# Kernel tuning notes

Hardware: AMD Instinct MI355X
Metric: run time of the kernel (lower is better)

Reference implementation:

```python
import jax, jax.numpy as jnp
import numpy as np

N = 100000   # nodes
E = 500000   # edges
H = 128      # h_dim
TAU = 1.0    # gumbel-softmax temperature (module default)


def setup_inputs() -> dict:
    key = jax.random.key(0)
    k = jax.random.split(key, 6)
    h = jax.random.normal(k[0], (N, H), dtype=jnp.float32)
    W1 = jax.random.normal(k[1], (2 * H, H // 2), dtype=jnp.float32) / np.float32(np.sqrt(2 * H))
    b1 = jnp.zeros((H // 2,), dtype=jnp.float32)
    W2 = jax.random.normal(k[2], (H // 2, 1), dtype=jnp.float32) / np.float32(np.sqrt(H // 2))
    b2 = jnp.zeros((1,), dtype=jnp.float32)
    u = jax.random.uniform(k[3], (E, 2), dtype=jnp.float32, minval=1e-6, maxval=1.0)
    edge_index = jax.random.randint(k[4], (2, E), 0, N, dtype=jnp.int32)
    return {"h": h, "W1": W1, "b1": b1, "W2": W2, "b2": b2, "u": u, "edge_index": edge_index}


def reference(h, W1, b1, W2, b2, u, edge_index):
    row, col = edge_index[0], edge_index[1]
    # gather endpoint features and concat: [E, 2H]
    edge_feat = jnp.concatenate([h[row], h[col]], axis=-1)
    # 2-layer MLP scorer -> per-edge logit [E]
    hid = jax.nn.relu(edge_feat @ W1 + b1)
    logits = (hid @ W2 + b2)[:, 0]
    # binary gumbel-softmax over [keep-logit=0, logit]
    samp_logits = jnp.stack([jnp.zeros_like(logits), logits], axis=-1)  # [E, 2]
    g = -jnp.log(-jnp.log(u))  # gumbel noise from uniform
    y_soft = jax.nn.softmax((samp_logits + g) / TAU, axis=-1)
    # hard=True straight-through
    idx = jnp.argmax(y_soft, axis=-1)
    y_hard = jax.nn.one_hot(idx, 2, dtype=y_soft.dtype)
    y = y_hard - jax.lax.stop_gradient(y_soft) + y_soft
    weights = y[:, 1]
    return (weights, logits)
```

## Files before the change

kernel.cpp:

```cpp
#include <hip/hip_runtime.h>
#include <math.h>

#define NN 100000
#define NE 500000

__global__ __launch_bounds__(256)
void node_proj(const float* __restrict__ h, const float* __restrict__ W1,
               const float* __restrict__ b1, float* __restrict__ AB, int nnodes)
{
    __shared__ float lh[64 * 132];

    const int t   = threadIdx.x;
    const int tj  = t & 15;
    const int tnf = t >> 4;
    const int n0  = blockIdx.x * 64;

#pragma unroll
    for (int i = 0; i < 8; ++i) {
        int flat = i * 256 + t;
        int nl = flat >> 5;
        int c  = flat & 31;
        int ng = n0 + nl;
        float4 v = make_float4(0.f, 0.f, 0.f, 0.f);
        if (ng < nnodes) v = *(const float4*)&h[(size_t)ng * 128 + c * 4];
        *(float4*)&lh[nl * 132 + c * 4] = v;
    }
    __syncthreads();

    const float* wa_base = W1 + tj * 4;
    const float* wb_base = W1 + 128 * 64 + tj * 4;

    float acc[4][8];
    {
        float4 bv = *(const float4*)&b1[tj * 4];
#pragma unroll
        for (int r = 0; r < 4; ++r) {
            acc[r][0] = bv.x; acc[r][1] = bv.y; acc[r][2] = bv.z; acc[r][3] = bv.w;
            acc[r][4] = 0.f;  acc[r][5] = 0.f;  acc[r][6] = 0.f;  acc[r][7] = 0.f;
        }
    }

    float4 A0[4], B0[4], A1[4], B1[4];
#pragma unroll
    for (int kk = 0; kk < 4; ++kk) {
        A0[kk] = *(const float4*)&wa_base[kk * 64];
        B0[kk] = *(const float4*)&wb_base[kk * 64];
    }

#define LOAD_W(AX, BX, K4)                                              \
    _Pragma("unroll")                                                   \
    for (int kk = 0; kk < 4; ++kk) {                                    \
        AX[kk] = *(const float4*)&wa_base[((K4) * 4 + kk) * 64];        \
        BX[kk] = *(const float4*)&wb_base[((K4) * 4 + kk) * 64];        \
    }

#define COMPUTE(AX, BX, K4)                                             \
    {                                                                   \
        float4 hv[4];                                                   \
        _Pragma("unroll")                                               \
        for (int r = 0; r < 4; ++r)                                     \
            hv[r] = *(const float4*)&lh[(tnf + 16 * r) * 132 + (K4) * 4]; \
        _Pragma("unroll")                                               \
        for (int kk = 0; kk < 4; ++kk) {                                \
            float4 wa = AX[kk], wb = BX[kk];                            \
            _Pragma("unroll")                                           \
            for (int r = 0; r < 4; ++r) {                               \
                float hk = (kk == 0) ? hv[r].x : (kk == 1) ? hv[r].y    \
                         : (kk == 2) ? hv[r].z : hv[r].w;               \
                acc[r][0] += hk * wa.x;                                 \
                acc[r][1] += hk * wa.y;                                 \
                acc[r][2] += hk * wa.z;                                 \
                acc[r][3] += hk * wa.w;                                 \
                acc[r][4] += hk * wb.x;                                 \
                acc[r][5] += hk * wb.y;                                 \
                acc[r][6] += hk * wb.z;                                 \
                acc[r][7] += hk * wb.w;                                 \
            }                                                           \
        }                                                               \
    }

#pragma unroll 1
    for (int k4 = 0; k4 < 30; k4 += 2) {
        LOAD_W(A1, B1, k4 + 1)
        COMPUTE(A0, B0, k4)
        LOAD_W(A0, B0, k4 + 2)
        COMPUTE(A1, B1, k4 + 1)
    }
    LOAD_W(A1, B1, 31)
    COMPUTE(A0, B0, 30)
    COMPUTE(A1, B1, 31)

#undef LOAD_W
#undef COMPUTE

#pragma unroll
    for (int r = 0; r < 4; ++r) {
        int ng = n0 + tnf + 16 * r;
        if (ng >= nnodes) continue;
        float* orow = AB + (size_t)ng * 128;
        *(float4*)&orow[tj * 4]      = make_float4(acc[r][0], acc[r][1], acc[r][2], acc[r][3]);
        *(float4*)&orow[64 + tj * 4] = make_float4(acc[r][4], acc[r][5], acc[r][6], acc[r][7]);
    }
}

__global__ __launch_bounds__(256)
void edge_sample(const float* __restrict__ AB, const float* __restrict__ W2,
                 const float* __restrict__ b2, const float* __restrict__ u,
                 const int* __restrict__ ei, float* __restrict__ out)
{
    int t = threadIdx.x;
    int l = t & 15;
    int e = blockIdx.x * 16 + (t >> 4);

    int row = ei[e];
    int col = ei[NE + e];

    float4 a = *(const float4*)&AB[(size_t)row * 128 + l * 4];
    float4 b = *(const float4*)&AB[(size_t)col * 128 + 64 + l * 4];
    float4 w = *(const float4*)&W2[l * 4];

    float h0 = fmaxf(a.x + b.x, 0.f);
    float h1 = fmaxf(a.y + b.y, 0.f);
    float h2 = fmaxf(a.z + b.z, 0.f);
    float h3 = fmaxf(a.w + b.w, 0.f);

    float p = h0 * w.x + h1 * w.y + h2 * w.z + h3 * w.w;
    p += __shfl_xor(p, 1);
    p += __shfl_xor(p, 2);
    p += __shfl_xor(p, 4);
    p += __shfl_xor(p, 8);

    if (l == 0) {
        float logit = p + b2[0];
        float u0 = u[2 * e];
        float u1 = u[2 * e + 1];
        float g0 = -logf(-logf(u0));
        float g1 = -logf(-logf(u1));
        out[e]      = (logit + g1 > g0) ? 1.0f : 0.0f;
        out[NE + e] = logit;
    }
}

__global__ __launch_bounds__(256)
void edge_direct(const float* __restrict__ h, const float* __restrict__ W1,
                 const float* __restrict__ b1, const float* __restrict__ W2,
                 const float* __restrict__ b2, const float* __restrict__ u,
                 const int* __restrict__ ei, float* __restrict__ out)
{
    int t = threadIdx.x;
    int l = t & 15;
    int e = blockIdx.x * 16 + (t >> 4);

    int row = ei[e];
    int col = ei[NE + e];

    float a0 = 0.f, a1 = 0.f, a2 = 0.f, a3 = 0.f;
    const float* hr = h + (size_t)row * 128;
    const float* hc = h + (size_t)col * 128;

    for (int k4 = 0; k4 < 32; ++k4) {
        float4 hv = *(const float4*)&hr[k4 * 4];
#pragma unroll
        for (int kk = 0; kk < 4; ++kk) {
            float4 wr = *(const float4*)&W1[(k4 * 4 + kk) * 64 + l * 4];
            float hval = (&hv.x)[kk];
            a0 += hval * wr.x; a1 += hval * wr.y; a2 += hval * wr.z; a3 += hval * wr.w;
        }
    }
    for (int k4 = 0; k4 < 32; ++k4) {
        float4 hv = *(const float4*)&hc[k4 * 4];
#pragma unroll
        for (int kk = 0; kk < 4; ++kk) {
            float4 wr = *(const float4*)&W1[(128 + k4 * 4 + kk) * 64 + l * 4];
            float hval = (&hv.x)[kk];
            a0 += hval * wr.x; a1 += hval * wr.y; a2 += hval * wr.z; a3 += hval * wr.w;
        }
    }
    float4 bb = *(const float4*)&b1[l * 4];
    float4 w  = *(const float4*)&W2[l * 4];
    float h0 = fmaxf(a0 + bb.x, 0.f);
    float h1 = fmaxf(a1 + bb.y, 0.f);
    float h2 = fmaxf(a2 + bb.z, 0.f);
    float h3 = fmaxf(a3 + bb.w, 0.f);

    float p = h0 * w.x + h1 * w.y + h2 * w.z + h3 * w.w;
    p += __shfl_xor(p, 1);
    p += __shfl_xor(p, 2);
    p += __shfl_xor(p, 4);
    p += __shfl_xor(p, 8);

    if (l == 0) {
        float logit = p + b2[0];
        float u0 = u[2 * e];
        float u1 = u[2 * e + 1];
        float g0 = -logf(-logf(u0));
        float g1 = -logf(-logf(u1));
        out[e]      = (logit + g1 > g0) ? 1.0f : 0.0f;
        out[NE + e] = logit;
    }
}

extern "C" void kernel_launch(void* const* d_in, const int* in_sizes, int n_in,
                              void* d_out, int out_size, void* d_ws, size_t ws_size,
                              hipStream_t stream)
{
    const float* h  = (const float*)d_in[0];
    const float* W1 = (const float*)d_in[1];
    const float* b1 = (const float*)d_in[2];
    const float* W2 = (const float*)d_in[3];
    const float* b2 = (const float*)d_in[4];
    const float* u  = (const float*)d_in[5];
    const int*   ei = (const int*)d_in[6];
    float* out = (float*)d_out;

    const size_t need = (size_t)NN * 128 * sizeof(float);
    if (ws_size >= need) {
        float* AB = (float*)d_ws;
        int nblocks = (NN + 63) / 64;
        node_proj<<<nblocks, 256, 0, stream>>>(h, W1, b1, AB, NN);
        edge_sample<<<NE / 16, 256, 0, stream>>>(AB, W2, b2, u, ei, out);
    } else {
        edge_direct<<<NE / 16, 256, 0, stream>>>(h, W1, b1, W2, b2, u, ei, out);
    }
}
```

Before: 104.6 us.

## Use bf16 MFMA for node projection with split weights and fp32 fallback near threshold

Replaces the fp32 node projection with a bf16 MFMA kernel: W1 is prepacked into high/low bf16 halves in MFMA fragment layout, while h is truncated to bf16. To guard the hard sample decision against the resulting error, the edge kernel recomputes the logit in full fp32 from h whenever the decision margin is under 0.02. This adds a prepack launch and divergent recompute work on borderline edges. The logits output is left with bf16-level error on most edges, which could break a tight tolerance.

```diff
diff --git a/kernel.cpp b/kernel.cpp
--- a/kernel.cpp
+++ b/kernel.cpp
@@ -3,6 +3,173 @@
 
 #define NN 100000
 #define NE 500000
+
+typedef short bf16x8 __attribute__((ext_vector_type(8)));
+typedef float f32x4  __attribute__((ext_vector_type(4)));
+
+static __device__ __forceinline__ unsigned short f2bf_rne(float x) {
+    unsigned int u = __builtin_bit_cast(unsigned int, x);
+    unsigned int r = u + 0x7fffu + ((u >> 16) & 1u);
+    return (unsigned short)(r >> 16);
+}
+static __device__ __forceinline__ float bf2f(unsigned short b) {
+    return __builtin_bit_cast(float, (unsigned int)b << 16);
+}
+
+__global__ __launch_bounds__(256)
+void prepack_w(const float* __restrict__ W1, unsigned short* __restrict__ WPh,
+               unsigned short* __restrict__ WPl)
+{
+    int idx = blockIdx.x * 256 + threadIdx.x;
+    int e  = idx & 7;
+    int l  = (idx >> 3) & 63;
+    int kt = (idx >> 9) & 3;
+    int jt = idx >> 11;
+    int k = kt * 32 + (l >> 4) * 8 + e;
+    int j = jt * 16 + (l & 15);
+    float w = (j < 64) ? W1[k * 64 + j] : W1[(128 + k) * 64 + (j - 64)];
+    unsigned short hb = f2bf_rne(w);
+    unsigned short lb = f2bf_rne(w - bf2f(hb));
+    WPh[idx] = hb;
+    WPl[idx] = lb;
+}
+
+__global__ __launch_bounds__(256)
+void mfma_proj(const float* __restrict__ h, const unsigned short* __restrict__ WPh,
+               const unsigned short* __restrict__ WPl, const float* __restrict__ b1,
+               float* __restrict__ AB, int nnodes)
+{
+    const int t  = threadIdx.x;
+    const int wv = t >> 6;
+    const int l  = t & 63;
+    const int lr = l & 15;
+    const int q  = l >> 4;
+    const int n0 = blockIdx.x * 64 + wv * 16;
+    const int arow = n0 + lr;
+    const bool aval = (arow < nnodes);
+
+    bf16x8 ah[4];
+    const float* hrow = h + (size_t)arow * 128;
+#pragma unroll
+    for (int kt = 0; kt < 4; ++kt) {
+        float4 x0 = make_float4(0.f, 0.f, 0.f, 0.f);
+        float4 x1 = make_float4(0.f, 0.f, 0.f, 0.f);
+        if (aval) {
+            x0 = *(const float4*)&hrow[kt * 32 + q * 8];
+            x1 = *(const float4*)&hrow[kt * 32 + q * 8 + 4];
+        }
+        float xs[8] = {x0.x, x0.y, x0.z, x0.w, x1.x, x1.y, x1.z, x1.w};
+        union { bf16x8 v; unsigned short u[8]; } H;
+#pragma unroll
+        for (int e = 0; e < 8; ++e)
+            H.u[e] = (unsigned short)(__builtin_bit_cast(unsigned int, xs[e]) >> 16);
+        ah[kt] = H.v;
+    }
+
+    const int drow = n0 + q * 4;
+
+#pragma unroll
+    for (int jt = 0; jt < 8; ++jt) {
+        f32x4 acc = {0.f, 0.f, 0.f, 0.f};
+#pragma unroll
+        for (int kt = 0; kt < 4; ++kt) {
+            const int fb = ((jt * 4 + kt) * 64 + l) * 8;
+            bf16x8 bh = *(const bf16x8*)(WPh + fb);
+            bf16x8 bl = *(const bf16x8*)(WPl + fb);
+            acc = __builtin_amdgcn_mfma_f32_16x16x32_bf16(ah[kt], bh, acc, 0, 0, 0);
+            acc = __builtin_amdgcn_mfma_f32_16x16x32_bf16(ah[kt], bl, acc, 0, 0, 0);
+        }
+        const int j = jt * 16 + lr;
+        const float bias = (jt < 4) ? b1[j] : 0.f;
+#pragma unroll
+        for (int r = 0; r < 4; ++r) {
+            int n = drow + r;
+            if (n < nnodes) AB[(size_t)n * 128 + j] = acc[r] + bias;
+        }
+    }
+}
+
+__global__ __launch_bounds__(256)
+void edge_sample(const float* __restrict__ AB, const float* __restrict__ h,
+                 const float* __restrict__ W1, const float* __restrict__ b1,
+                 const float* __restrict__ W2, const float* __restrict__ b2,
+                 const float* __restrict__ u, const int* __restrict__ ei,
+                 float* __restrict__ out)
+{
+    int t = threadIdx.x;
+    int l = t & 15;
+    int e = blockIdx.x * 16 + (t >> 4);
+
+    int row = ei[e];
+    int col = ei[NE + e];
+
+    float4 a = *(const float4*)&AB[(size_t)row * 128 + l * 4];
+    float4 b = *(const float4*)&AB[(size_t)col * 128 + 64 + l * 4];
+    float4 w = *(const float4*)&W2[l * 4];
+
+    float h0 = fmaxf(a.x + b.x, 0.f);
+    float h1 = fmaxf(a.y + b.y, 0.f);
+    float h2 = fmaxf(a.z + b.z, 0.f);
+    float h3 = fmaxf(a.w + b.w, 0.f);
+
+    float p = h0 * w.x + h1 * w.y + h2 * w.z + h3 * w.w;
+    p += __shfl_xor(p, 1);
+    p += __shfl_xor(p, 2);
+    p += __shfl_xor(p, 4);
+    p += __shfl_xor(p, 8);
+
+    float logit = p + b2[0];
+    float g0 = 0.f, g1 = 0.f, dec = 0.f;
+    if (l == 0) {
+        float u0 = u[2 * e];
+        float u1 = u[2 * e + 1];
+        g0 = -logf(-logf(u0));
+        g1 = -logf(-logf(u1));
+        dec = (logit + g1) - g0;
+    }
+    int base = (t & 63) & ~15;
+    float dec_b = __shfl(dec, base);
+
+    if (fabsf(dec_b) < 0.02f) {
+        float4 bb = *(const float4*)&b1[l * 4];
+        float a0 = bb.x, a1 = bb.y, a2 = bb.z, a3 = bb.w;
+        const float* hr = h + (size_t)row * 128;
+        const float* hc = h + (size_t)col * 128;
+        for (int k4 = 0; k4 < 32; ++k4) {
+            float4 hv = *(const float4*)&hr[k4 * 4];
+#pragma unroll
+            for (int kk = 0; kk < 4; ++kk) {
+                float4 wr = *(const float4*)&W1[(k4 * 4 + kk) * 64 + l * 4];
+                float hval = (&hv.x)[kk];
+                a0 += hval * wr.x; a1 += hval * wr.y;
+                a2 += hval * wr.z; a3 += hval * wr.w;
+            }
+        }
+        for (int k4 = 0; k4 < 32; ++k4) {
+            float4 hv = *(const float4*)&hc[k4 * 4];
+#pragma unroll
+            for (int kk = 0; kk < 4; ++kk) {
+                float4 wr = *(const float4*)&W1[(128 + k4 * 4 + kk) * 64 + l * 4];
+                float hval = (&hv.x)[kk];
+                a0 += hval * wr.x; a1 += hval * wr.y;
+                a2 += hval * wr.z; a3 += hval * wr.w;
+            }
+        }
+        float r0 = fmaxf(a0, 0.f), r1 = fmaxf(a1, 0.f);
+        float r2 = fmaxf(a2, 0.f), r3 = fmaxf(a3, 0.f);
+        float p2 = r0 * w.x + r1 * w.y + r2 * w.z + r3 * w.w;
+        p2 += __shfl_xor(p2, 1);
+        p2 += __shfl_xor(p2, 2);
+        p2 += __shfl_xor(p2, 4);
+        p2 += __shfl_xor(p2, 8);
+        logit = p2 + b2[0];
+    }
+
+    if (l == 0) {
+        out[e]      = (logit + g1 > g0) ? 1.0f : 0.0f;
+        out[NE + e] = logit;
+    }
+}
 
 __global__ __launch_bounds__(256)
 void node_proj(const float* __restrict__ h, const float* __restrict__ W1,
@@ -104,7 +271,8 @@
 }
 
 __global__ __launch_bounds__(256)
-void edge_sample(const float* __restrict__ AB, const float* __restrict__ W2,
+void edge_direct(const float* __restrict__ h, const float* __restrict__ W1,
+                 const float* __restrict__ b1, const float* __restrict__ W2,
                  const float* __restrict__ b2, const float* __restrict__ u,
                  const int* __restrict__ ei, float* __restrict__ out)
 {
@@ -115,14 +283,34 @@
     int row = ei[e];
     int col = ei[NE + e];
 
-    float4 a = *(const float4*)&AB[(size_t)row * 128 + l * 4];
-    float4 b = *(const float4*)&AB[(size_t)col * 128 + 64 + l * 4];
-    float4 w = *(const float4*)&W2[l * 4];
-
-    float h0 = fmaxf(a.x + b.x, 0.f);
-    float h1 = fmaxf(a.y + b.y, 0.f);
-    float h2 = fmaxf(a.z + b.z, 0.f);
-    float h3 = fmaxf(a.w + b.w, 0.f);
+    float a0 = 0.f, a1 = 0.f, a2 = 0.f, a3 = 0.f;
+    const float* hr = h + (size_t)row * 128;
+    const float* hc = h + (size_t)col * 128;
+
+    for (int k4 = 0; k4 < 32; ++k4) {
+        float4 hv = *(const float4*)&hr[k4 * 4];
+#pragma unroll
+        for (int kk = 0; kk < 4; ++kk) {
+            float4 wr = *(const float4*)&W1[(k4 * 4 + kk) * 64 + l * 4];
+            float hval = (&hv.x)[kk];
+            a0 += hval * wr.x; a1 += hval * wr.y; a2 += hval * wr.z; a3 += hval * wr.w;
+        }
+    }
+    for (int k4 = 0; k4 < 32; ++k4) {
+        float4 hv = *(const float4*)&hc[k4 * 4];
+#pragma unroll
+        for (int kk = 0; kk < 4; ++kk) {
+            float4 wr = *(const float4*)&W1[(128 + k4 * 4 + kk) * 64 + l * 4];
+            float hval = (&hv.x)[kk];
+            a0 += hval * wr.x; a1 += hval * wr.y; a2 += hval * wr.z; a3 += hval * wr.w;
+        }
+    }
+    float4 bb = *(const float4*)&b1[l * 4];
+    float4 w  = *(const float4*)&W2[l * 4];
+    float h0 = fmaxf(a0 + bb.x, 0.f);
+    float h1 = fmaxf(a1 + bb.y, 0.f);
+    float h2 = fmaxf(a2 + bb.z, 0.f);
+    float h3 = fmaxf(a3 + bb.w, 0.f);
 
     float p = h0 * w.x + h1 * w.y + h2 * w.z + h3 * w.w;
     p += __shfl_xor(p, 1);
@@ -141,65 +329,6 @@
     }
 }
 
-__global__ __launch_bounds__(256)
-void edge_direct(const float* __restrict__ h, const float* __restrict__ W1,
-                 const float* __restrict__ b1, const float* __restrict__ W2,
-                 const float* __restrict__ b2, const float* __restrict__ u,
-                 const int* __restrict__ ei, float* __restrict__ out)
-{
-    int t = threadIdx.x;
-    int l = t & 15;
-    int e = blockIdx.x * 16 + (t >> 4);
-
-    int row = ei[e];
-    int col = ei[NE + e];
-
-    float a0 = 0.f, a1 = 0.f, a2 = 0.f, a3 = 0.f;
-    const float* hr = h + (size_t)row * 128;
-    const float* hc = h + (size_t)col * 128;
-
-    for (int k4 = 0; k4 < 32; ++k4) {
-        float4 hv = *(const float4*)&hr[k4 * 4];
-#pragma unroll
-        for (int kk = 0; kk < 4; ++kk) {
-            float4 wr = *(const float4*)&W1[(k4 * 4 + kk) * 64 + l * 4];
-            float hval = (&hv.x)[kk];
-            a0 += hval * wr.x; a1 += hval * wr.y; a2 += hval * wr.z; a3 += hval * wr.w;
-        }
-    }
-    for (int k4 = 0; k4 < 32; ++k4) {
-        float4 hv = *(const float4*)&hc[k4 * 4];
-#pragma unroll
-        for (int kk = 0; kk < 4; ++kk) {
-            float4 wr = *(const float4*)&W1[(128 + k4 * 4 + kk) * 64 + l * 4];
-            float hval = (&hv.x)[kk];
-            a0 += hval * wr.x; a1 += hval * wr.y; a2 += hval * wr.z; a3 += hval * wr.w;
-        }
-    }
-    float4 bb = *(const float4*)&b1[l * 4];
-    float4 w  = *(const float4*)&W2[l * 4];
-    float h0 = fmaxf(a0 + bb.x, 0.f);
-    float h1 = fmaxf(a1 + bb.y, 0.f);
-    float h2 = fmaxf(a2 + bb.z, 0.f);
-    float h3 = fmaxf(a3 + bb.w, 0.f);
-
-    float p = h0 * w.x + h1 * w.y + h2 * w.z + h3 * w.w;
-    p += __shfl_xor(p, 1);
-    p += __shfl_xor(p, 2);
-    p += __shfl_xor(p, 4);
-    p += __shfl_xor(p, 8);
-
-    if (l == 0) {
-        float logit = p + b2[0];
-        float u0 = u[2 * e];
-        float u1 = u[2 * e + 1];
-        float g0 = -logf(-logf(u0));
-        float g1 = -logf(-logf(u1));
-        out[e]      = (logit + g1 > g0) ? 1.0f : 0.0f;
-        out[NE + e] = logit;
-    }
-}
-
 extern "C" void kernel_launch(void* const* d_in, const int* in_sizes, int n_in,
                               void* d_out, int out_size, void* d_ws, size_t ws_size,
                               hipStream_t stream)
@@ -213,12 +342,19 @@
     const int*   ei = (const int*)d_in[6];
     float* out = (float*)d_out;
 
-    const size_t need = (size_t)NN * 128 * sizeof(float);
-    if (ws_size >= need) {
-        float* AB = (float*)d_ws;
-        int nblocks = (NN + 63) / 64;
-        node_proj<<<nblocks, 256, 0, stream>>>(h, W1, b1, AB, NN);
-        edge_sample<<<NE / 16, 256, 0, stream>>>(AB, W2, b2, u, ei, out);
+    const size_t ab_bytes = (size_t)NN * 128 * sizeof(float);
+    const size_t wp_bytes = 2u * 16384u * sizeof(unsigned short);
+    float* AB = (float*)d_ws;
+
+    if (ws_size >= ab_bytes + wp_bytes) {
+        unsigned short* WPh = (unsigned short*)((char*)d_ws + ab_bytes);
+        unsigned short* WPl = WPh + 16384;
+        prepack_w<<<64, 256, 0, stream>>>(W1, WPh, WPl);
+        mfma_proj<<<(NN + 63) / 64, 256, 0, stream>>>(h, WPh, WPl, b1, AB, NN);
+        edge_sample<<<NE / 16, 256, 0, stream>>>(AB, h, W1, b1, W2, b2, u, ei, out);
+    } else if (ws_size >= ab_bytes) {
+        node_proj<<<(NN + 63) / 64, 256, 0, stream>>>(h, W1, b1, AB, NN);
+        edge_sample<<<NE / 16, 256, 0, stream>>>(AB, h, W1, b1, W2, b2, u, ei, out);
     } else {
         edge_direct<<<NE / 16, 256, 0, stream>>>(h, W1, b1, W2, b2, u, ei, out);
     }
```

New measurement: 115.8 us. +10.7%, slower.
